# Optimization experiments

Hardware: AMD Instinct MI355X
Metric: run time of the kernel (lower is better)

## Reference

```python
import jax, jax.numpy as jnp
import numpy as np

N = 10000        # nodes
F_IN = 128       # node features (data.num_node_features)
OUT = 16         # out_channels
H = 32           # attention heads
C1 = 4 * OUT     # hidden per-head dim (4*out_channels)
E = 80000        # directed edges
EPS = 1e-5       # BatchNorm eps
NEG = 0.2        # GATConv LeakyReLU negative_slope


def _gat(x, src, dst, W, a_s, a_d, b, n, C):
    # PyG GATConv, shared lin, concat=False (mean over heads)
    h = (x @ W).reshape(n, H, C)                    # [n,H,C]
    e_src = jnp.sum(h * a_s, -1)                    # [n,H] (alpha from x_j)
    e_dst = jnp.sum(h * a_d, -1)                    # [n,H] (alpha from x_i)
    e = jax.nn.leaky_relu(e_src[src] + e_dst[dst], NEG)     # [E',H]
    m = jax.ops.segment_max(e, dst, num_segments=n)         # segment softmax
    p = jnp.exp(e - m[dst])
    z = jax.ops.segment_sum(p, dst, num_segments=n)
    alpha = p / z[dst]
    out = jax.ops.segment_sum(alpha[:, :, None] * h[src], dst, num_segments=n)
    return out.mean(1) + b                          # mean over heads + bias


def _bn(x, g, b, m, v):  # eval-mode BatchNorm1d (running stats)
    return (x - m) * g / jnp.sqrt(v + EPS) + b


def setup_inputs():
    k = jax.random.split(jax.random.key(0), 40)
    rn = lambda i, s, sc=0.1: jax.random.normal(k[i], s, jnp.float32) * sc
    d = {"x": jax.random.normal(k[0], (N, F_IN), jnp.float32),
         "edge_index": jax.random.randint(k[1], (2, E), 0, N, jnp.int32)}
    # 4 GATConv layers
    d.update(W1=rn(2, (F_IN, H * C1)), as1=rn(3, (H, C1)), ad1=rn(4, (H, C1)), b1=rn(5, (C1,)))
    d.update(W2=rn(6, (C1, H * OUT)), as2=rn(7, (H, OUT)), ad2=rn(8, (H, OUT)), b2=rn(9, (OUT,)))
    d.update(W3=rn(10, (F_IN, H * C1)), as3=rn(11, (H, C1)), ad3=rn(12, (H, C1)), b3=rn(13, (C1,)))
    d.update(W4=rn(14, (C1, H * OUT)), as4=rn(15, (H, OUT)), ad4=rn(16, (H, OUT)), b4=rn(17, (OUT,)))
    # ResidualNetwork(1 block): 1x1 Conv1d over L=1 == matmul
    d.update(rwa=rn(18, (F_IN, OUT)), rba=rn(19, (OUT,)),
             bn1g=jnp.ones(OUT), bn1b=jnp.zeros(OUT), bn1m=rn(20, (OUT,)), bn1v=jnp.abs(rn(21, (OUT,))) + 1.0,
             rwb=rn(22, (OUT, OUT)), rbb=rn(23, (OUT,)),
             bn2g=jnp.ones(OUT), bn2b=jnp.zeros(OUT), bn2m=rn(24, (OUT,)), bn2v=jnp.abs(rn(25, (OUT,))) + 1.0,
             wsc=rn(26, (F_IN, OUT)), bsc=rn(27, (OUT,)),
             bnsg=jnp.ones(OUT), bnsb=jnp.zeros(OUT), bnsm=rn(28, (OUT,)), bnsv=jnp.abs(rn(29, (OUT,))) + 1.0,
             wfc=rn(30, (OUT, OUT)), bfc=rn(31, (OUT,)))
    return d


def reference(x, edge_index, W1, as1, ad1, b1, W2, as2, ad2, b2,
              W3, as3, ad3, b3, W4, as4, ad4, b4,
              rwa, rba, bn1g, bn1b, bn1m, bn1v, rwb, rbb, bn2g, bn2b, bn2m, bn2v,
              wsc, bsc, bnsg, bnsb, bnsm, bnsv, wfc, bfc):
    n = x.shape[0]
    loops = jnp.arange(n, dtype=edge_index.dtype)  # add_self_loops=True
    s2t_src = jnp.concatenate([edge_index[0], loops])  # flow source_to_target
    s2t_dst = jnp.concatenate([edge_index[1], loops])
    t2s_src = jnp.concatenate([edge_index[1], loops])  # flow target_to_source
    t2s_dst = jnp.concatenate([edge_index[0], loops])
    # dropout in original is unassigned (no-op); eval mode assumed
    x_s = jax.nn.elu(_gat(x, s2t_src, s2t_dst, W1, as1, ad1, b1, n, C1))
    x_in = jax.nn.elu(_gat(x_s, s2t_src, s2t_dst, W2, as2, ad2, b2, n, OUT))
    x_t = jax.nn.elu(_gat(x, t2s_src, t2s_dst, W3, as3, ad3, b3, n, C1))
    x_out = jax.nn.elu(_gat(x_t, t2s_src, t2s_dst, W4, as4, ad4, b4, n, OUT))
    # ResidualNetwork: block + identity avg-pool (L=1) + fc
    h = jax.nn.relu(_bn(x @ rwa + rba, bn1g, bn1b, bn1m, bn1v))
    h = _bn(h @ rwb + rbb, bn2g, bn2b, bn2m, bn2v)
    sc = _bn(x @ wsc + bsc, bnsg, bnsb, bnsm, bnsv)
    x_self = jax.nn.relu(h + sc) @ wfc + bfc
    return (x_in, x_out, x_self)
```

## Files before the change

### kernel.cpp

```cpp
#include <hip/hip_runtime.h>
#include <stdint.h>

__device__ __forceinline__ float bf2f(unsigned short u) {
  union { unsigned int i; float f; } v; v.i = ((unsigned int)u) << 16; return v.f;
}
__device__ __forceinline__ unsigned short f2bf(float f) {
  union { float f; unsigned int i; } v; v.f = f;
  unsigned int i = v.i;
  unsigned int r = (i + 0x7fffu + ((i >> 16) & 1u)) >> 16;
  return (unsigned short)r;
}

typedef __bf16 bf16x8 __attribute__((ext_vector_type(8)));
typedef float f32x4 __attribute__((ext_vector_type(4)));
union ABfrag { int4 i4; bf16x8 v; };

#if __has_builtin(__builtin_amdgcn_cvt_pk_fp8_f32) && __has_builtin(__builtin_amdgcn_cvt_pk_f32_fp8)
#define HW_FP8 1
#else
#define HW_FP8 0
#endif

__device__ __forceinline__ unsigned char f2fp8_sw(float f) {
  union { float f; unsigned int u; } v; v.f = f;
  unsigned int s = (v.u >> 24) & 0x80;
  float a = fabsf(f);
  if (a >= 448.f) return (unsigned char)(s | 0x7E);
  v.f = a;
  int ex = (int)(v.u >> 23);
  unsigned int man = v.u & 0x7FFFFFu;
  if (ex >= 121) {
    unsigned int val = ((unsigned int)(ex - 120) << 3) | (man >> 20);
    unsigned int rem = man & 0xFFFFFu;
    if (rem > 0x80000u || (rem == 0x80000u && (val & 1))) val++;
    if (val > 0x7E) val = 0x7E;
    return (unsigned char)(s | val);
  }
  int q = (int)(a * 512.f + 0.5f);
  if (q > 8) q = 8;
  return (unsigned char)(s | (unsigned int)q);
}
__device__ __forceinline__ float fp8dec_sw(unsigned char c) {
  unsigned int e = (c >> 3) & 15u, m = c & 7u;
  float v;
  if (e) { union { unsigned int u; float f; } x; x.u = ((e + 120) << 23) | (m << 20); v = x.f; }
  else v = (float)m * 0.001953125f;
  return (c & 0x80) ? -v : v;
}
__device__ __forceinline__ unsigned char f2fp8(float f) {
#if HW_FP8
  int v = __builtin_amdgcn_cvt_pk_fp8_f32(f, f, 0, false);
  return (unsigned char)(v & 0xFF);
#else
  return f2fp8_sw(f);
#endif
}
__device__ __forceinline__ void dec16(int4 g, float o[16]) {
#if HW_FP8
  { auto p = __builtin_amdgcn_cvt_pk_f32_fp8(g.x, false); o[0]=p[0]; o[1]=p[1]; }
  { auto p = __builtin_amdgcn_cvt_pk_f32_fp8(g.x, true ); o[2]=p[0]; o[3]=p[1]; }
  { auto p = __builtin_amdgcn_cvt_pk_f32_fp8(g.y, false); o[4]=p[0]; o[5]=p[1]; }
  { auto p = __builtin_amdgcn_cvt_pk_f32_fp8(g.y, true ); o[6]=p[0]; o[7]=p[1]; }
  { auto p = __builtin_amdgcn_cvt_pk_f32_fp8(g.z, false); o[8]=p[0]; o[9]=p[1]; }
  { auto p = __builtin_amdgcn_cvt_pk_f32_fp8(g.z, true ); o[10]=p[0]; o[11]=p[1]; }
  { auto p = __builtin_amdgcn_cvt_pk_f32_fp8(g.w, false); o[12]=p[0]; o[13]=p[1]; }
  { auto p = __builtin_amdgcn_cvt_pk_f32_fp8(g.w, true ); o[14]=p[0]; o[15]=p[1]; }
#else
  unsigned int w[4] = {(unsigned)g.x, (unsigned)g.y, (unsigned)g.z, (unsigned)g.w};
#pragma unroll
  for (int d = 0; d < 4; ++d)
#pragma unroll
    for (int b = 0; b < 4; ++b) o[d*4+b] = fp8dec_sw((unsigned char)((w[d] >> (b*8)) & 0xFF));
#endif
}

__device__ __forceinline__ float lrelu_clamp(float e) {
  e = (e > 0.f) ? e : 0.2f * e;
  return fminf(e, 80.f);
}

__global__ __launch_bounds__(256) void k_detect(const unsigned int* __restrict__ x, int* flag) {
  __shared__ int cnt;
  if (threadIdx.x == 0) cnt = 0;
  __syncthreads();
  int c = 0;
  for (int i = threadIdx.x; i < 1024; i += 256) {
    unsigned int lo = x[i] & 0xFFFFu;
    int ex = (int)((lo >> 7) & 0xFF);
    if (ex >= 100 && ex <= 140) c++;
  }
  atomicAdd(&cnt, c);
  __syncthreads();
  if (threadIdx.x == 0) flag[0] = (cnt > 600) ? 1 : 0;
}

struct PrepDesc {
  const void* csrc[32]; float* cdst[32]; int cn[32];
  const void* x; float* xc; unsigned short* xp;
  const void* W1; const void* W2; const void* W3; const void* W4;
  unsigned short* P1; unsigned short* P2; unsigned short* P3; unsigned short* P4;
  int* degAB;
  int nxb, xtotal, ctotal, ndeg2;
};
__global__ __launch_bounds__(256) void k_prep(PrepDesc d, const int* __restrict__ flag) {
  int isbf = *flag;
  int b = blockIdx.x;
  if (b < d.nxb) {
    int i = b * 256 + threadIdx.x;
    if (i < d.xtotal) {
      float v = isbf ? bf2f(((const unsigned short*)d.x)[i]) : ((const float*)d.x)[i];
      d.xc[i] = v;
      int row = i >> 7, c = i & 127;
      int tm = row >> 4, mr = row & 15;
      int s = c >> 5, quad = (c >> 3) & 3, j = c & 7;
      size_t idx = (((size_t)tm * 4 + s) * 64 + quad * 16 + mr) * 8 + j;
      d.xp[idx] = f2bf(v);
    }
    return;
  }
  b -= d.nxb;
  if (b < 288) {
    int u = b * 256 + threadIdx.x;
    const void* W; unsigned short* P; int K, N, lu;
    if (u < 32768)      { W = d.W1; P = d.P1; K = 128; N = 2048; lu = u; }
    else if (u < 36864) { W = d.W2; P = d.P2; K = 64;  N = 512;  lu = u - 32768; }
    else if (u < 69632) { W = d.W3; P = d.P3; K = 128; N = 2048; lu = u - 36864; }
    else                { W = d.W4; P = d.P4; K = 64;  N = 512;  lu = u - 69632; }
    int ksteps = K >> 5;
    int g = lu / (ksteps * 64);
    int rem = lu - g * (ksteps * 64);
    int s = rem >> 6, lane = rem & 63;
    int mr = lane & 15, quad = lane >> 4;
    int col = g * 16 + mr;
    int kbase = s * 32 + quad * 8;
#pragma unroll
    for (int j = 0; j < 8; ++j) {
      size_t src = (size_t)(kbase + j) * N + col;
      float v = isbf ? bf2f(((const unsigned short*)W)[src]) : ((const float*)W)[src];
      P[(size_t)lu * 8 + j] = f2bf(v);
    }
    return;
  }
  b -= 288;
  if (b < 4) {
    for (int idx = b * 256 + threadIdx.x; idx < d.ctotal; idx += 4 * 256) {
      int t = 0, off = idx;
      while (off >= d.cn[t]) { off -= d.cn[t]; ++t; }
      float v = isbf ? bf2f(((const unsigned short*)d.csrc[t])[off])
                     : ((const float*)d.csrc[t])[off];
      d.cdst[t][off] = v;
    }
    return;
  }
  b -= 4;
  for (int idx = b * 256 + threadIdx.x; idx < d.ndeg2; idx += 8 * 256) d.degAB[idx] = 0;
}

__global__ __launch_bounds__(256) void k_deg_count(const int* __restrict__ ei, int* degA, int* degB, int E) {
  int e = blockIdx.x * 256 + threadIdx.x;
  if (e < E) { atomicAdd(&degA[ei[E + e]], 1); atomicAdd(&degB[ei[e]], 1); }
}
__global__ __launch_bounds__(1024) void k_exscan2(const int* __restrict__ degA, const int* __restrict__ degB,
                                                  int* __restrict__ rowA, int* __restrict__ rowB,
                                                  int* __restrict__ colA, int* __restrict__ colB,
                                                  int* __restrict__ curA, int* __restrict__ curB, int n) {
  const int* deg = (blockIdx.x == 0) ? degA : degB;
  int* row = (blockIdx.x == 0) ? rowA : rowB;
  int* colx = (blockIdx.x == 0) ? colA : colB;
  int* curx = (blockIdx.x == 0) ? curA : curB;
  __shared__ int wsum[16], wbase[16];
  __shared__ int carry;
  if (threadIdx.x == 0) carry = 0;
  __syncthreads();
  int lane = threadIdx.x & 63, w = threadIdx.x >> 6;
  int chunks = (n + 1023) >> 10;
  for (int ch = 0; ch < chunks; ++ch) {
    int i = (ch << 10) + threadIdx.x;
    int v = (i < n) ? deg[i] : 0;
    int sc = v;
#pragma unroll
    for (int o = 1; o < 64; o <<= 1) { int t = __shfl_up(sc, o); if (lane >= o) sc += t; }
    if (lane == 63) wsum[w] = sc;
    __syncthreads();
    if (threadIdx.x < 16) {
      int v2 = wsum[threadIdx.x], s2 = v2;
#pragma unroll
      for (int o = 1; o < 16; o <<= 1) { int t = __shfl_up(s2, o); if (lane >= o) s2 += t; }
      wbase[threadIdx.x] = s2 - v2;
      if (threadIdx.x == 15) wsum[15] = s2;
    }
    __syncthreads();
    if (i < n) {
      int rv = carry + wbase[w] + (sc - v) + i;
      row[i] = rv;
      colx[rv] = i;
      curx[i] = rv + 1;
    }
    __syncthreads();
    if (threadIdx.x == 0) carry += wsum[15];
    __syncthreads();
  }
  if (threadIdx.x == 0) row[n] = carry + n;
}
__global__ __launch_bounds__(256) void k_scatter(const int* __restrict__ ei, int* colA, int* colB,
                                                 int* curA, int* curB, int E) {
  int e = blockIdx.x * 256 + threadIdx.x;
  if (e < E) {
    int s = ei[e], d = ei[E + e];
    colA[atomicAdd(&curA[d], 1)] = s;
    colB[atomicAdd(&curB[s], 1)] = d;
  }
}

union SMem {
  unsigned char tile[4][16][64];
  struct { float xs[16][128]; float ha[16][16]; float tt[16][16]; } res;
};

template<int CH, int KSTEPS>
__device__ __forceinline__ void mm_es_body(int vblk,
    const unsigned short* __restrict__ Ap, const unsigned short* __restrict__ Bp,
    unsigned char* __restrict__ C, const float* __restrict__ a_s, const float* __restrict__ a_d,
    float* __restrict__ es, float* __restrict__ ed, int N, SMem* sm) {
  int wid = threadIdx.x >> 6;
  int wg = vblk * 4 + wid;
  int ntiles = N >> 6;
  int tm = wg / ntiles, tn = wg % ntiles;
  int lane = threadIdx.x & 63;
  int mr = lane & 15, quad = lane >> 4;
  const unsigned short* ap = Ap + ((size_t)tm * KSTEPS) * 512 + lane * 8;
  const unsigned short* bp = Bp + ((size_t)tn * 4 * KSTEPS) * 512 + lane * 8;
  f32x4 acc[4];
#pragma unroll
  for (int i = 0; i < 4; i++) acc[i] = (f32x4){0.f, 0.f, 0.f, 0.f};
#pragma unroll
  for (int s = 0; s < KSTEPS; ++s) {
    ABfrag a; a.i4 = *(const int4*)(ap + s * 512);
#pragma unroll
    for (int nt = 0; nt < 4; ++nt) {
      ABfrag b; b.i4 = *(const int4*)(bp + (size_t)(nt * KSTEPS + s) * 512);
      acc[nt] = __builtin_amdgcn_mfma_f32_16x16x32_bf16(a.v, b.v, acc[nt], 0, 0, 0);
    }
  }
#pragma unroll
  for (int nt = 0; nt < 4; ++nt)
#pragma unroll
    for (int r = 0; r < 4; ++r)
      sm->tile[wid][quad * 4 + r][nt * 16 + mr] = f2fp8(acc[nt][r]);
  __syncthreads();
  {
    int r16 = lane >> 2, seg = lane & 3;
    int4 val = *(const int4*)&sm->tile[wid][r16][seg * 16];
    *(int4*)(C + (size_t)(tm * 16 + r16) * N + tn * 64 + seg * 16) = val;
  }
  if (CH == 64) {
    float pes[4] = {0.f,0.f,0.f,0.f}, ped[4] = {0.f,0.f,0.f,0.f};
    const float* asr = a_s + tn * 64;
    const float* adr = a_d + tn * 64;
#pragma unroll
    for (int nt = 0; nt < 4; ++nt) {
      float ws = asr[nt * 16 + mr], wd = adr[nt * 16 + mr];
#pragma unroll
      for (int r = 0; r < 4; ++r) { pes[r] += acc[nt][r] * ws; ped[r] += acc[nt][r] * wd; }
    }
#pragma unroll
    for (int m = 1; m < 16; m <<= 1)
#pragma unroll
      for (int r = 0; r < 4; ++r) {
        pes[r] += __shfl_xor(pes[r], m);
        ped[r] += __shfl_xor(ped[r], m);
      }
    if (mr == 0) {
#pragma unroll
      for (int r = 0; r < 4; ++r) {
        int row = tm * 16 + quad * 4 + r;
        es[row * 32 + tn] = pes[r];
        ed[row * 32 + tn] = ped[r];
      }
    }
  } else {
    float pes[4][4], ped[4][4];
#pragma unroll
    for (int nt = 0; nt < 4; ++nt) {
      float ws = a_s[(tn * 4 + nt) * 16 + mr];
      float wd = a_d[(tn * 4 + nt) * 16 + mr];
#pragma unroll
      for (int r = 0; r < 4; ++r) { pes[nt][r] = acc[nt][r] * ws; ped[nt][r] = acc[nt][r] * wd; }
    }
#pragma unroll
    for (int m = 1; m < 16; m <<= 1)
#pragma unroll
      for (int nt = 0; nt < 4; ++nt)
#pragma unroll
        for (int r = 0; r < 4; ++r) {
          pes[nt][r] += __shfl_xor(pes[nt][r], m);
          ped[nt][r] += __shfl_xor(ped[nt][r], m);
        }
    if (mr == 0) {
#pragma unroll
      for (int nt = 0; nt < 4; ++nt)
#pragma unroll
        for (int r = 0; r < 4; ++r) {
          int row = tm * 16 + quad * 4 + r;
          es[row * 32 + tn * 4 + nt] = pes[nt][r];
          ed[row * 32 + tn * 4 + nt] = ped[nt][r];
        }
    }
  }
}

struct MM13Desc {
  const unsigned short* Ap;
  const unsigned short* B1; const unsigned short* B3;
  unsigned char* C1; unsigned char* C3;
  const float* as1; const float* ad1; const float* as3; const float* ad3;
  float* es1; float* ed1; float* es3; float* ed3;
  int mmblks;
  const float* xc;
  const float* rp[20];
  void* outbase; size_t eoff; int n;
  const int* flag;
};
__global__ __launch_bounds__(256) void k_mm13res(MM13Desc d) {
  __shared__ SMem sm;
  int b = blockIdx.x;
  if (b < d.mmblks) {
    mm_es_body<64,4>(b, d.Ap, d.B1, d.C1, d.as1, d.ad1, d.es1, d.ed1, 2048, &sm);
    return;
  }
  b -= d.mmblks;
  if (b < d.mmblks) {
    mm_es_body<64,4>(b, d.Ap, d.B3, d.C3, d.as3, d.ad3, d.es3, d.ed3, 2048, &sm);
    return;
  }
  b -= d.mmblks;
  int nodebase = b * 16;
  for (int t = threadIdx.x; t < 16 * 128; t += 256)
    sm.res.xs[t >> 7][t & 127] = d.xc[(size_t)(nodebase + (t >> 7)) * 128 + (t & 127)];
  __syncthreads();
  int ni = threadIdx.x >> 4, c = threadIdx.x & 15;
  const float* rwa = d.rp[0]; const float* rba = d.rp[1];
  const float* bn1g = d.rp[2]; const float* bn1b = d.rp[3];
  const float* bn1m = d.rp[4]; const float* bn1v = d.rp[5];
  const float* rwb = d.rp[6]; const float* rbb = d.rp[7];
  const float* bn2g = d.rp[8]; const float* bn2b = d.rp[9];
  const float* bn2m = d.rp[10]; const float* bn2v = d.rp[11];
  const float* wsc = d.rp[12]; const float* bsc = d.rp[13];
  const float* bnsg = d.rp[14]; const float* bnsb = d.rp[15];
  const float* bnsm = d.rp[16]; const float* bnsv = d.rp[17];
  const float* wfc = d.rp[18]; const float* bfc = d.rp[19];
  float ya = 0.f, ysc = 0.f;
  for (int k = 0; k < 128; ++k) {
    float xv = sm.res.xs[ni][k];
    ya  += xv * rwa[k * 16 + c];
    ysc += xv * wsc[k * 16 + c];
  }
  ya += rba[c]; ysc += bsc[c];
  float s1 = bn1g[c] * rsqrtf(bn1v[c] + 1e-5f);
  ya = (ya - bn1m[c]) * s1 + bn1b[c];
  ya = fmaxf(ya, 0.f);
  float ss = bnsg[c] * rsqrtf(bnsv[c] + 1e-5f);
  ysc = (ysc - bnsm[c]) * ss + bnsb[c];
  sm.res.ha[ni][c] = ya;
  __syncthreads();
  float h2 = rbb[c];
  for (int k = 0; k < 16; ++k) h2 += sm.res.ha[ni][k] * rwb[k * 16 + c];
  float s2 = bn2g[c] * rsqrtf(bn2v[c] + 1e-5f);
  h2 = (h2 - bn2m[c]) * s2 + bn2b[c];
  sm.res.tt[ni][c] = fmaxf(h2 + ysc, 0.f);
  __syncthreads();
  float o = bfc[c];
  for (int k = 0; k < 16; ++k) o += sm.res.tt[ni][k] * wfc[k * 16 + c];
  size_t oo = d.eoff + (size_t)(nodebase + ni) * 16 + c;
  if (*d.flag) ((unsigned short*)d.outbase)[oo] = f2bf(o);
  else         ((float*)d.outbase)[oo] = o;
}

__global__ __launch_bounds__(256) void k_g64(const unsigned char* __restrict__ h1,
                                             const unsigned char* __restrict__ h3,
                                             const float* __restrict__ es1, const float* __restrict__ ed1,
                                             const float* __restrict__ es3, const float* __restrict__ ed3,
                                             const int* __restrict__ rowA, const int* __restrict__ colA,
                                             const int* __restrict__ rowB, const int* __restrict__ colB,
                                             const float* __restrict__ b1, const float* __restrict__ b3,
                                             unsigned short* __restrict__ xsp, unsigned short* __restrict__ xtp,
                                             int n, int gb) {
  int b = blockIdx.x;
  const unsigned char* h; const float *es, *ed, *bias; const int *rowp, *col; unsigned short* outp;
  if (b < gb) { h = h1; es = es1; ed = ed1; rowp = rowA; col = colA; bias = b1; outp = xsp; }
  else { b -= gb; h = h3; es = es3; ed = ed3; rowp = rowB; col = colB; bias = b3; outp = xtp; }
  int wid = threadIdx.x >> 6, lane = threadIdx.x & 63;
  int i = b * 4 + wid;
  if (i >= n) return;
  int hd0 = lane >> 2, hd1 = 16 + hd0;
  float e0 = ed[i * 32 + hd0];
  float e1 = ed[i * 32 + hd1];
  int beg = rowp[i], end = rowp[i + 1];
  int deg = end - beg;
  int colv = (lane < deg) ? col[beg + lane] : 0;
  float acc0[16], acc1[16];
#pragma unroll
  for (int k = 0; k < 16; ++k) { acc0[k] = 0.f; acc1[k] = 0.f; }
  float Z0 = 0.f, Z1 = 0.f;
  for (int j = 0; j < deg; ++j) {
    int s = (j < 64) ? __shfl(colv, j) : col[beg + j];
    const int4* hp = (const int4*)(h + (size_t)s * 2048);
    int4 g0 = hp[lane];
    int4 g1 = hp[64 + lane];
    float q0 = __expf(lrelu_clamp(es[s * 32 + hd0] + e0));
    float q1 = __expf(lrelu_clamp(es[s * 32 + hd1] + e1));
    Z0 += q0; Z1 += q1;
    float d0[16], d1[16];
    dec16(g0, d0); dec16(g1, d1);
#pragma unroll
    for (int k = 0; k < 16; ++k) { acc0[k] += q0 * d0[k]; acc1[k] += q1 * d1[k]; }
  }
  float zi0 = 1.0f / Z0, zi1 = 1.0f / Z1;
  float v[16];
#pragma unroll
  for (int k = 0; k < 16; ++k) v[k] = acc0[k] * zi0 + acc1[k] * zi1;
#pragma unroll
  for (int m = 4; m < 64; m <<= 1)
#pragma unroll
    for (int k = 0; k < 16; ++k) v[k] += __shfl_xor(v[k], m);
  if (lane < 4) {
    int tm = i >> 4, mr = i & 15;
    unsigned short ob[16];
#pragma unroll
    for (int k = 0; k < 16; ++k) {
      float t = v[k] * (1.f / 32.f) + bias[lane * 16 + k];
      t = (t > 0.f) ? t : (__expf(t) - 1.f);
      ob[k] = f2bf(t);
    }
    int s0 = lane >> 1;
#pragma unroll
    for (int g2 = 0; g2 < 2; ++g2) {
      size_t idx = (((size_t)tm * 2 + s0) * 64 + ((lane & 1) * 2 + g2) * 16 + mr) * 8;
      *(int4*)(outp + idx) = *(const int4*)(ob + g2 * 8);
    }
  }
}

__global__ __launch_bounds__(256) void k_mm24(const unsigned short* __restrict__ xsp,
                                              const unsigned short* __restrict__ xtp,
                                              const unsigned short* __restrict__ W2p,
                                              const unsigned short* __restrict__ W4p,
                                              unsigned char* __restrict__ h2, unsigned char* __restrict__ h4,
                                              const float* __restrict__ as2, const float* __restrict__ ad2,
                                              const float* __restrict__ as4, const float* __restrict__ ad4,
                                              float* __restrict__ es2, float* __restrict__ ed2,
                                              float* __restrict__ es4, float* __restrict__ ed4,
                                              int mmblks) {
  __shared__ SMem sm;
  int b = blockIdx.x;
  if (b < mmblks)
    mm_es_body<16,2>(b, xsp, W2p, h2, as2, ad2, es2, ed2, 512, &sm);
  else
    mm_es_body<16,2>(b - mmblks, xtp, W4p, h4, as4, ad4, es4, ed4, 512, &sm);
}

__global__ __launch_bounds__(256) void k_g16(const unsigned char* __restrict__ h2,
                                             const unsigned char* __restrict__ h4,
                                             const float* __restrict__ es2, const float* __restrict__ ed2,
                                             const float* __restrict__ es4, const float* __restrict__ ed4,
                                             const int* __restrict__ rowA, const int* __restrict__ colA,
                                             const int* __restrict__ rowB, const int* __restrict__ colB,
                                             const float* __restrict__ b2, const float* __restrict__ b4,
                                             void* __restrict__ outbase, int n, int gb,
                                             const int* __restrict__ flag) {
  int b = blockIdx.x;
  const unsigned char* h; const float *es, *ed, *bias; const int *rowp, *col; size_t eoff;
  if (b < gb) { h = h2; es = es2; ed = ed2; rowp = rowA; col = colA; bias = b2; eoff = 0; }
  else { b -= gb; h = h4; es = es4; ed = ed4; rowp = rowB; col = colB; bias = b4; eoff = (size_t)n * 16; }
  int wid = threadIdx.x >> 6, lane = threadIdx.x & 63;
  int i = b * 4 + wid;
  if (i >= n) return;
  int hh = lane & 31, j2 = lane >> 5;
  float ev = ed[i * 32 + hh];
  int beg = rowp[i], end = rowp[i + 1];
  int deg = end - beg;
  int colv = (lane < deg) ? col[beg + lane] : 0;
  float acc[16];
#pragma unroll
  for (int k = 0; k < 16; ++k) acc[k] = 0.f;
  float Z = 0.f;
  for (int j = j2; j < deg; j += 2) {
    int s = (j < 64) ? __shfl(colv, j) : col[beg + j];
    int4 g = ((const int4*)(h + (size_t)s * 512))[hh];
    float q = __expf(lrelu_clamp(es[s * 32 + hh] + ev));
    Z += q;
    float d[16];
    dec16(g, d);
#pragma unroll
    for (int k = 0; k < 16; ++k) acc[k] += q * d[k];
  }
  Z += __shfl_xor(Z, 32);
  float zi = 1.0f / Z;
  float v[16];
#pragma unroll
  for (int k = 0; k < 16; ++k) v[k] = acc[k] * zi;
#pragma unroll
  for (int m = 1; m < 64; m <<= 1)
#pragma unroll
    for (int k = 0; k < 16; ++k) v[k] += __shfl_xor(v[k], m);
  if (lane == 0) {
    int isbf = *flag;
    if (isbf) {
      unsigned short ob[16];
#pragma unroll
      for (int k = 0; k < 16; ++k) {
        float t = v[k] * (1.f / 32.f) + bias[k];
        t = (t > 0.f) ? t : (__expf(t) - 1.f);
        ob[k] = f2bf(t);
      }
      unsigned short* o = (unsigned short*)outbase + eoff + (size_t)i * 16;
      *(int4*)o = *(const int4*)ob;
      *(int4*)(o + 8) = *(const int4*)(ob + 8);
    } else {
      float* o = (float*)outbase + eoff + (size_t)i * 16;
#pragma unroll
      for (int k = 0; k < 16; ++k) {
        float t = v[k] * (1.f / 32.f) + bias[k];
        t = (t > 0.f) ? t : (__expf(t) - 1.f);
        o[k] = t;
      }
    }
  }
}

extern "C" void kernel_launch(void* const* d_in, const int* in_sizes, int n_in,
                              void* d_out, int out_size, void* d_ws, size_t ws_size,
                              hipStream_t stream) {
  const int n = in_sizes[0] / 128;
  const int E = in_sizes[1] / 2;
  const int* ei = (const int*)d_in[1];

  char* wsp = (char*)d_ws; size_t off = 0;
  auto alloc = [&](size_t bytes) -> void* {
    void* p = wsp + off; off = (off + bytes + 255) & ~(size_t)255; return p;
  };
  int* flag = (int*)alloc(4);
  float* xc = (float*)alloc((size_t)n * 128 * 4);
  unsigned short* xp = (unsigned short*)alloc((size_t)n * 128 * 2);
  unsigned short* W1p = (unsigned short*)alloc((size_t)2048 * 128 * 2);
  unsigned short* W2p = (unsigned short*)alloc((size_t)512 * 64 * 2);
  unsigned short* W3p = (unsigned short*)alloc((size_t)2048 * 128 * 2);
  unsigned short* W4p = (unsigned short*)alloc((size_t)512 * 64 * 2);
  unsigned char* h1 = (unsigned char*)alloc((size_t)n * 2048);
  unsigned char* h3 = (unsigned char*)alloc((size_t)n * 2048);
  unsigned char* h2 = (unsigned char*)alloc((size_t)n * 512);
  unsigned char* h4 = (unsigned char*)alloc((size_t)n * 512);
  float* es1 = (float*)alloc((size_t)n * 32 * 4);
  float* ed1 = (float*)alloc((size_t)n * 32 * 4);
  float* es3 = (float*)alloc((size_t)n * 32 * 4);
  float* ed3 = (float*)alloc((size_t)n * 32 * 4);
  float* es2 = (float*)alloc((size_t)n * 32 * 4);
  float* ed2 = (float*)alloc((size_t)n * 32 * 4);
  float* es4 = (float*)alloc((size_t)n * 32 * 4);
  float* ed4 = (float*)alloc((size_t)n * 32 * 4);
  unsigned short* xsp = (unsigned short*)alloc((size_t)n * 64 * 2);
  unsigned short* xtp = (unsigned short*)alloc((size_t)n * 64 * 2);
  int* rowA = (int*)alloc((size_t)(n + 1) * 4);
  int* rowB = (int*)alloc((size_t)(n + 1) * 4);
  int* colA = (int*)alloc((size_t)(E + n) * 4);
  int* colB = (int*)alloc((size_t)(E + n) * 4);
  int* degAB = (int*)alloc((size_t)2 * n * 4);
  int* degA = degAB, * degB = degAB + n;
  int* curA = (int*)alloc((size_t)n * 4);
  int* curB = (int*)alloc((size_t)n * 4);

  static const int cidx[32] = {3,4,5, 7,8,9, 11,12,13, 15,16,17,
                               18,19,20,21,22,23,24,25,26,27,28,29,
                               30,31,32,33,34,35,36,37};
  PrepDesc pd;
  float* canon[38] = {nullptr};
  pd.ctotal = 0;
  for (int t = 0; t < 32; ++t) {
    int ii = cidx[t];
    canon[ii] = (float*)alloc((size_t)in_sizes[ii] * 4);
    pd.csrc[t] = d_in[ii];
    pd.cdst[t] = canon[ii];
    pd.cn[t] = in_sizes[ii];
    pd.ctotal += in_sizes[ii];
  }
  pd.x = d_in[0]; pd.xc = xc; pd.xp = xp;
  pd.W1 = d_in[2]; pd.W2 = d_in[6]; pd.W3 = d_in[10]; pd.W4 = d_in[14];
  pd.P1 = W1p; pd.P2 = W2p; pd.P3 = W3p; pd.P4 = W4p;
  pd.degAB = degAB;
  pd.nxb = (n * 128 + 255) / 256;
  pd.xtotal = n * 128;
  pd.ndeg2 = 2 * n;
  (void)ws_size; (void)n_in; (void)out_size;

  k_detect<<<1, 256, 0, stream>>>((const unsigned int*)d_in[0], flag);
  k_prep<<<pd.nxb + 288 + 4 + 8, 256, 0, stream>>>(pd, flag);

  k_deg_count<<<(E + 255) / 256, 256, 0, stream>>>(ei, degA, degB, E);
  k_exscan2<<<2, 1024, 0, stream>>>(degA, degB, rowA, rowB, colA, colB, curA, curB, n);
  k_scatter<<<(E + 255) / 256, 256, 0, stream>>>(ei, colA, colB, curA, curB, E);

  const int mt = n / 16;
  const int mmblks64 = mt * 32 / 4;
  const int mmblks16 = mt * 8 / 4;
  const int gb = (n + 3) / 4;

  MM13Desc md;
  md.Ap = xp; md.B1 = W1p; md.B3 = W3p; md.C1 = h1; md.C3 = h3;
  md.as1 = canon[3]; md.ad1 = canon[4]; md.as3 = canon[11]; md.ad3 = canon[12];
  md.es1 = es1; md.ed1 = ed1; md.es3 = es3; md.ed3 = ed3;
  md.mmblks = mmblks64;
  md.xc = xc;
  for (int t = 0; t < 20; ++t) md.rp[t] = canon[18 + t];
  md.outbase = d_out; md.eoff = (size_t)2 * n * 16; md.n = n; md.flag = flag;
  k_mm13res<<<2 * mmblks64 + n / 16, 256, 0, stream>>>(md);

  k_g64<<<2 * gb, 256, 0, stream>>>(h1, h3, es1, ed1, es3, ed3,
                                    rowA, colA, rowB, colB,
                                    canon[5], canon[13], xsp, xtp, n, gb);
  k_mm24<<<2 * mmblks16, 256, 0, stream>>>(xsp, xtp, W2p, W4p, h2, h4,
                                           canon[7], canon[8], canon[15], canon[16],
                                           es2, ed2, es4, ed4, mmblks16);
  k_g16<<<2 * gb, 256, 0, stream>>>(h2, h4, es2, ed2, es4, ed4,
                                    rowA, colA, rowB, colB,
                                    canon[9], canon[17], d_out, n, gb, flag);
}
```

Measured before the change: 328.5 us.

## Fold CSR build kernels into neighbours, prefetch gathers, use packed FMA

Moves the degree-zeroing into k_detect, the degree counting into k_prep, and the CSR scatter into extra blocks of k_mm13res, cutting two kernel launches. The gather loops in k_g64 and k_g16 now software-prefetch the next neighbour's features and score so loads overlap compute. The accumulation uses two-wide float vectors with elementwise FMA to encourage packed math. The risk is extra register pressure from the prefetch buffers. Correctness also relies on stream ordering: the scatter blocks must not race with the matmul blocks, which is fine because they touch disjoint data.

```diff
diff --git a/kernel.cpp b/kernel.cpp
--- a/kernel.cpp
+++ b/kernel.cpp
@@ -13,6 +13,7 @@
 
 typedef __bf16 bf16x8 __attribute__((ext_vector_type(8)));
 typedef float f32x4 __attribute__((ext_vector_type(4)));
+typedef float f32x2 __attribute__((ext_vector_type(2)));
 union ABfrag { int4 i4; bf16x8 v; };
 
 #if __has_builtin(__builtin_amdgcn_cvt_pk_fp8_f32) && __has_builtin(__builtin_amdgcn_cvt_pk_f32_fp8)
@@ -55,22 +56,26 @@
   return f2fp8_sw(f);
 #endif
 }
-__device__ __forceinline__ void dec16(int4 g, float o[16]) {
+__device__ __forceinline__ void dec16p(int4 g, f32x2 o[8]) {
 #if HW_FP8
-  { auto p = __builtin_amdgcn_cvt_pk_f32_fp8(g.x, false); o[0]=p[0]; o[1]=p[1]; }
-  { auto p = __builtin_amdgcn_cvt_pk_f32_fp8(g.x, true ); o[2]=p[0]; o[3]=p[1]; }
-  { auto p = __builtin_amdgcn_cvt_pk_f32_fp8(g.y, false); o[4]=p[0]; o[5]=p[1]; }
-  { auto p = __builtin_amdgcn_cvt_pk_f32_fp8(g.y, true ); o[6]=p[0]; o[7]=p[1]; }
-  { auto p = __builtin_amdgcn_cvt_pk_f32_fp8(g.z, false); o[8]=p[0]; o[9]=p[1]; }
-  { auto p = __builtin_amdgcn_cvt_pk_f32_fp8(g.z, true ); o[10]=p[0]; o[11]=p[1]; }
-  { auto p = __builtin_amdgcn_cvt_pk_f32_fp8(g.w, false); o[12]=p[0]; o[13]=p[1]; }
-  { auto p = __builtin_amdgcn_cvt_pk_f32_fp8(g.w, true ); o[14]=p[0]; o[15]=p[1]; }
+  o[0] = __builtin_amdgcn_cvt_pk_f32_fp8(g.x, false);
+  o[1] = __builtin_amdgcn_cvt_pk_f32_fp8(g.x, true);
+  o[2] = __builtin_amdgcn_cvt_pk_f32_fp8(g.y, false);
+  o[3] = __builtin_amdgcn_cvt_pk_f32_fp8(g.y, true);
+  o[4] = __builtin_amdgcn_cvt_pk_f32_fp8(g.z, false);
+  o[5] = __builtin_amdgcn_cvt_pk_f32_fp8(g.z, true);
+  o[6] = __builtin_amdgcn_cvt_pk_f32_fp8(g.w, false);
+  o[7] = __builtin_amdgcn_cvt_pk_f32_fp8(g.w, true);
 #else
   unsigned int w[4] = {(unsigned)g.x, (unsigned)g.y, (unsigned)g.z, (unsigned)g.w};
 #pragma unroll
-  for (int d = 0; d < 4; ++d)
-#pragma unroll
-    for (int b = 0; b < 4; ++b) o[d*4+b] = fp8dec_sw((unsigned char)((w[d] >> (b*8)) & 0xFF));
+  for (int d = 0; d < 4; ++d) {
+    unsigned int x = w[d];
+    o[d * 2 + 0] = (f32x2){fp8dec_sw((unsigned char)(x & 0xFF)),
+                           fp8dec_sw((unsigned char)((x >> 8) & 0xFF))};
+    o[d * 2 + 1] = (f32x2){fp8dec_sw((unsigned char)((x >> 16) & 0xFF)),
+                           fp8dec_sw((unsigned char)((x >> 24) & 0xFF))};
+  }
 #endif
 }
 
@@ -79,19 +84,24 @@
   return fminf(e, 80.f);
 }
 
-__global__ __launch_bounds__(256) void k_detect(const unsigned int* __restrict__ x, int* flag) {
-  __shared__ int cnt;
-  if (threadIdx.x == 0) cnt = 0;
-  __syncthreads();
-  int c = 0;
-  for (int i = threadIdx.x; i < 1024; i += 256) {
-    unsigned int lo = x[i] & 0xFFFFu;
-    int ex = (int)((lo >> 7) & 0xFF);
-    if (ex >= 100 && ex <= 140) c++;
-  }
-  atomicAdd(&cnt, c);
-  __syncthreads();
-  if (threadIdx.x == 0) flag[0] = (cnt > 600) ? 1 : 0;
+__global__ __launch_bounds__(256) void k_detect(const unsigned int* __restrict__ x, int* flag,
+                                                int* __restrict__ degAB, int ndeg2) {
+  if (blockIdx.x == 0) {
+    __shared__ int cnt;
+    if (threadIdx.x == 0) cnt = 0;
+    __syncthreads();
+    int c = 0;
+    for (int i = threadIdx.x; i < 1024; i += 256) {
+      unsigned int lo = x[i] & 0xFFFFu;
+      int ex = (int)((lo >> 7) & 0xFF);
+      if (ex >= 100 && ex <= 140) c++;
+    }
+    atomicAdd(&cnt, c);
+    __syncthreads();
+    if (threadIdx.x == 0) flag[0] = (cnt > 600) ? 1 : 0;
+    return;
+  }
+  for (int idx = (blockIdx.x - 1) * 256 + threadIdx.x; idx < ndeg2; idx += 8 * 256) degAB[idx] = 0;
 }
 
 struct PrepDesc {
@@ -100,7 +110,8 @@
   const void* W1; const void* W2; const void* W3; const void* W4;
   unsigned short* P1; unsigned short* P2; unsigned short* P3; unsigned short* P4;
   int* degAB;
-  int nxb, xtotal, ctotal, ndeg2;
+  const int* ei;
+  int nxb, xtotal, ctotal, E, nn;
 };
 __global__ __launch_bounds__(256) void k_prep(PrepDesc d, const int* __restrict__ flag) {
   int isbf = *flag;
@@ -153,13 +164,15 @@
     return;
   }
   b -= 4;
-  for (int idx = b * 256 + threadIdx.x; idx < d.ndeg2; idx += 8 * 256) d.degAB[idx] = 0;
-}
-
-__global__ __launch_bounds__(256) void k_deg_count(const int* __restrict__ ei, int* degA, int* degB, int E) {
-  int e = blockIdx.x * 256 + threadIdx.x;
-  if (e < E) { atomicAdd(&degA[ei[E + e]], 1); atomicAdd(&degB[ei[e]], 1); }
-}
+  {
+    int e = b * 256 + threadIdx.x;
+    if (e < d.E) {
+      atomicAdd(&d.degAB[d.ei[d.E + e]], 1);
+      atomicAdd(&d.degAB[d.nn + d.ei[e]], 1);
+    }
+  }
+}
+
 __global__ __launch_bounds__(1024) void k_exscan2(const int* __restrict__ degA, const int* __restrict__ degB,
                                                   int* __restrict__ rowA, int* __restrict__ rowB,
                                                   int* __restrict__ colA, int* __restrict__ colB,
@@ -202,15 +215,6 @@
   }
   if (threadIdx.x == 0) row[n] = carry + n;
 }
-__global__ __launch_bounds__(256) void k_scatter(const int* __restrict__ ei, int* colA, int* colB,
-                                                 int* curA, int* curB, int E) {
-  int e = blockIdx.x * 256 + threadIdx.x;
-  if (e < E) {
-    int s = ei[e], d = ei[E + e];
-    colA[atomicAdd(&curA[d], 1)] = s;
-    colB[atomicAdd(&curB[s], 1)] = d;
-  }
-}
 
 union SMem {
   unsigned char tile[4][16][64];
@@ -315,7 +319,8 @@
   unsigned char* C1; unsigned char* C3;
   const float* as1; const float* ad1; const float* as3; const float* ad3;
   float* es1; float* ed1; float* es3; float* ed3;
-  int mmblks;
+  int sblks, mmblks, resblks, E;
+  const int* ei; int* colA; int* colB; int* curA; int* curB;
   const float* xc;
   const float* rp[20];
   void* outbase; size_t eoff; int n;
@@ -324,6 +329,16 @@
 __global__ __launch_bounds__(256) void k_mm13res(MM13Desc d) {
   __shared__ SMem sm;
   int b = blockIdx.x;
+  if (b < d.sblks) {
+    int e = b * 256 + threadIdx.x;
+    if (e < d.E) {
+      int s = d.ei[e], dd = d.ei[d.E + e];
+      d.colA[atomicAdd(&d.curA[dd], 1)] = s;
+      d.colB[atomicAdd(&d.curB[s], 1)] = dd;
+    }
+    return;
+  }
+  b -= d.sblks;
   if (b < d.mmblks) {
     mm_es_body<64,4>(b, d.Ap, d.B1, d.C1, d.as1, d.ad1, d.es1, d.ed1, 2048, &sm);
     return;
@@ -398,32 +413,57 @@
   int beg = rowp[i], end = rowp[i + 1];
   int deg = end - beg;
   int colv = (lane < deg) ? col[beg + lane] : 0;
-  float acc0[16], acc1[16];
-#pragma unroll
-  for (int k = 0; k < 16; ++k) { acc0[k] = 0.f; acc1[k] = 0.f; }
+  f32x2 acc0[8], acc1[8];
+#pragma unroll
+  for (int k = 0; k < 8; ++k) { acc0[k] = (f32x2){0.f, 0.f}; acc1[k] = (f32x2){0.f, 0.f}; }
   float Z0 = 0.f, Z1 = 0.f;
+  int s0 = __shfl(colv, 0);
+  const int4* hp0 = (const int4*)(h + (size_t)s0 * 2048);
+  int4 ng0 = hp0[lane];
+  int4 ng1 = hp0[64 + lane];
+  float na = es[s0 * 32 + hd0];
+  float nb = es[s0 * 32 + hd1];
   for (int j = 0; j < deg; ++j) {
-    int s = (j < 64) ? __shfl(colv, j) : col[beg + j];
-    const int4* hp = (const int4*)(h + (size_t)s * 2048);
-    int4 g0 = hp[lane];
-    int4 g1 = hp[64 + lane];
-    float q0 = __expf(lrelu_clamp(es[s * 32 + hd0] + e0));
-    float q1 = __expf(lrelu_clamp(es[s * 32 + hd1] + e1));
+    int4 g0 = ng0, g1 = ng1;
+    float ea = na, eb = nb;
+    int jn = j + 1;
+    if (jn < deg) {
+      int sn = (jn < 64) ? __shfl(colv, jn) : col[beg + jn];
+      const int4* hq = (const int4*)(h + (size_t)sn * 2048);
+      ng0 = hq[lane];
+      ng1 = hq[64 + lane];
+      na = es[sn * 32 + hd0];
+      nb = es[sn * 32 + hd1];
+    }
+    float q0 = __expf(lrelu_clamp(ea + e0));
+    float q1 = __expf(lrelu_clamp(eb + e1));
     Z0 += q0; Z1 += q1;
-    float d0[16], d1[16];
-    dec16(g0, d0); dec16(g1, d1);
-#pragma unroll
-    for (int k = 0; k < 16; ++k) { acc0[k] += q0 * d0[k]; acc1[k] += q1 * d1[k]; }
+    f32x2 d0[8], d1[8];
+    dec16p(g0, d0); dec16p(g1, d1);
+    f32x2 q0v = (f32x2){q0, q0}, q1v = (f32x2){q1, q1};
+#pragma unroll
+    for (int k = 0; k < 8; ++k) {
+      acc0[k] = __builtin_elementwise_fma(q0v, d0[k], acc0[k]);
+      acc1[k] = __builtin_elementwise_fma(q1v, d1[k], acc1[k]);
+    }
   }
   float zi0 = 1.0f / Z0, zi1 = 1.0f / Z1;
-  float v[16];
-#pragma unroll
-  for (int k = 0; k < 16; ++k) v[k] = acc0[k] * zi0 + acc1[k] * zi1;
+  f32x2 zi0v = (f32x2){zi0, zi0}, zi1v = (f32x2){zi1, zi1};
+  f32x2 v2[8];
+#pragma unroll
+  for (int k = 0; k < 8; ++k)
+    v2[k] = __builtin_elementwise_fma(acc1[k], zi1v, acc0[k] * zi0v);
 #pragma unroll
   for (int m = 4; m < 64; m <<= 1)
 #pragma unroll
-    for (int k = 0; k < 16; ++k) v[k] += __shfl_xor(v[k], m);
+    for (int k = 0; k < 8; ++k) {
+      v2[k].x += __shfl_xor(v2[k].x, m);
+      v2[k].y += __shfl_xor(v2[k].y, m);
+    }
   if (lane < 4) {
+    float v[16];
+#pragma unroll
+    for (int k = 0; k < 8; ++k) { v[2 * k] = v2[k].x; v[2 * k + 1] = v2[k].y; }
     int tm = i >> 4, mr = i & 15;
     unsigned short ob[16];
 #pragma unroll
@@ -432,10 +472,10 @@
       t = (t > 0.f) ? t : (__expf(t) - 1.f);
       ob[k] = f2bf(t);
     }
-    int s0 = lane >> 1;
+    int s0w = lane >> 1;
 #pragma unroll
     for (int g2 = 0; g2 < 2; ++g2) {
-      size_t idx = (((size_t)tm * 2 + s0) * 64 + ((lane & 1) * 2 + g2) * 16 + mr) * 8;
+      size_t idx = (((size_t)tm * 2 + s0w) * 64 + ((lane & 1) * 2 + g2) * 16 + mr) * 8;
       *(int4*)(outp + idx) = *(const int4*)(ob + g2 * 8);
     }
   }
@@ -480,30 +520,51 @@
   int beg = rowp[i], end = rowp[i + 1];
   int deg = end - beg;
   int colv = (lane < deg) ? col[beg + lane] : 0;
-  float acc[16];
-#pragma unroll
-  for (int k = 0; k < 16; ++k) acc[k] = 0.f;
+  f32x2 acc[8];
+#pragma unroll
+  for (int k = 0; k < 8; ++k) acc[k] = (f32x2){0.f, 0.f};
   float Z = 0.f;
-  for (int j = j2; j < deg; j += 2) {
-    int s = (j < 64) ? __shfl(colv, j) : col[beg + j];
-    int4 g = ((const int4*)(h + (size_t)s * 512))[hh];
-    float q = __expf(lrelu_clamp(es[s * 32 + hh] + ev));
+  int j = j2;
+  int4 ng = (int4){0, 0, 0, 0};
+  float ne = 0.f;
+  if (j < deg) {
+    int s = __shfl(colv, j);
+    ng = ((const int4*)(h + (size_t)s * 512))[hh];
+    ne = es[s * 32 + hh];
+  }
+  for (; j < deg; j += 2) {
+    int4 g = ng; float ee = ne;
+    int jn = j + 2;
+    if (jn < deg) {
+      int sn = (jn < 64) ? __shfl(colv, jn) : col[beg + jn];
+      ng = ((const int4*)(h + (size_t)sn * 512))[hh];
+      ne = es[sn * 32 + hh];
+    }
+    float q = __expf(lrelu_clamp(ee + ev));
     Z += q;
-    float d[16];
-    dec16(g, d);
-#pragma unroll
-    for (int k = 0; k < 16; ++k) acc[k] += q * d[k];
+    f32x2 d[8];
+    dec16p(g, d);
+    f32x2 qv = (f32x2){q, q};
+#pragma unroll
+    for (int k = 0; k < 8; ++k) acc[k] = __builtin_elementwise_fma(qv, d[k], acc[k]);
   }
   Z += __shfl_xor(Z, 32);
   float zi = 1.0f / Z;
-  float v[16];
-#pragma unroll
-  for (int k = 0; k < 16; ++k) v[k] = acc[k] * zi;
+  f32x2 ziv = (f32x2){zi, zi};
+  f32x2 v2[8];
+#pragma unroll
+  for (int k = 0; k < 8; ++k) v2[k] = acc[k] * ziv;
 #pragma unroll
   for (int m = 1; m < 64; m <<= 1)
 #pragma unroll
-    for (int k = 0; k < 16; ++k) v[k] += __shfl_xor(v[k], m);
+    for (int k = 0; k < 8; ++k) {
+      v2[k].x += __shfl_xor(v2[k].x, m);
+      v2[k].y += __shfl_xor(v2[k].y, m);
+    }
   if (lane == 0) {
+    float v[16];
+#pragma unroll
+    for (int k = 0; k < 8; ++k) { v[2 * k] = v2[k].x; v[2 * k + 1] = v2[k].y; }
     int isbf = *flag;
     if (isbf) {
       unsigned short ob[16];
@@ -587,17 +648,18 @@
   pd.W1 = d_in[2]; pd.W2 = d_in[6]; pd.W3 = d_in[10]; pd.W4 = d_in[14];
   pd.P1 = W1p; pd.P2 = W2p; pd.P3 = W3p; pd.P4 = W4p;
   pd.degAB = degAB;
+  pd.ei = ei;
   pd.nxb = (n * 128 + 255) / 256;
   pd.xtotal = n * 128;
-  pd.ndeg2 = 2 * n;
+  pd.E = E;
+  pd.nn = n;
   (void)ws_size; (void)n_in; (void)out_size;
 
-  k_detect<<<1, 256, 0, stream>>>((const unsigned int*)d_in[0], flag);
-  k_prep<<<pd.nxb + 288 + 4 + 8, 256, 0, stream>>>(pd, flag);
-
-  k_deg_count<<<(E + 255) / 256, 256, 0, stream>>>(ei, degA, degB, E);
+  const int degblks = (E + 255) / 256;
+
+  k_detect<<<9, 256, 0, stream>>>((const unsigned int*)d_in[0], flag, degAB, 2 * n);
+  k_prep<<<pd.nxb + 288 + 4 + degblks, 256, 0, stream>>>(pd, flag);
   k_exscan2<<<2, 1024, 0, stream>>>(degA, degB, rowA, rowB, colA, colB, curA, curB, n);
-  k_scatter<<<(E + 255) / 256, 256, 0, stream>>>(ei, colA, colB, curA, curB, E);
 
   const int mt = n / 16;
   const int mmblks64 = mt * 32 / 4;
@@ -608,11 +670,12 @@
   md.Ap = xp; md.B1 = W1p; md.B3 = W3p; md.C1 = h1; md.C3 = h3;
   md.as1 = canon[3]; md.ad1 = canon[4]; md.as3 = canon[11]; md.ad3 = canon[12];
   md.es1 = es1; md.ed1 = ed1; md.es3 = es3; md.ed3 = ed3;
-  md.mmblks = mmblks64;
+  md.sblks = degblks; md.mmblks = mmblks64; md.resblks = mt; md.E = E;
+  md.ei = ei; md.colA = colA; md.colB = colB; md.curA = curA; md.curB = curB;
   md.xc = xc;
   for (int t = 0; t < 20; ++t) md.rp[t] = canon[18 + t];
   md.outbase = d_out; md.eoff = (size_t)2 * n * 16; md.n = n; md.flag = flag;
-  k_mm13res<<<2 * mmblks64 + n / 16, 256, 0, stream>>>(md);
+  k_mm13res<<<degblks + 2 * mmblks64 + mt, 256, 0, stream>>>(md);
 
   k_g64<<<2 * gb, 256, 0, stream>>>(h1, h3, es1, ed1, es3, ed3,
                                     rowA, colA, rowB, colB,
```

New measurement: 319.9 us. -2.6%, faster.
